# Kernel optimization log

Measured on AMD Instinct MI355X. Metric: run time of the kernel, lower is better.

## Reference

```python
import jax, jax.numpy as jnp
import numpy as np

NUM_NODES = 50000
IN_CH0 = 128
HEADS = 8
NUM_EDGES = 625000
IN_CH1 = 64


def setup_inputs() -> dict:
    key = jax.random.key(0)
    k0, k1, k2, k3 = jax.random.split(key, 4)
    x_0 = jax.random.normal(k0, (NUM_NODES, IN_CH0), dtype=jnp.float32)
    adjacency_0 = jax.random.randint(k1, (2, NUM_EDGES), 0, NUM_NODES, dtype=jnp.int64)
    x_1 = jax.random.normal(k2, (NUM_EDGES, IN_CH1), dtype=jnp.float32)
    # Xavier-uniform with relu gain, shape (2*C, heads)
    gain = float(np.sqrt(2.0))
    fan_in, fan_out = 2 * IN_CH0, HEADS
    bound = gain * np.sqrt(6.0 / (fan_in + fan_out))
    att_parameter = jax.random.uniform(k3, (2 * IN_CH0, HEADS), minval=-bound, maxval=bound, dtype=jnp.float32)
    return {"x_0": x_0, "adjacency_0": adjacency_0, "x_1": x_1, "att_parameter": att_parameter}


def reference(x_0, adjacency_0, x_1, att_parameter):
    # LiftLayer: gather source/target node feats, concat, small matmul, relu.
    source = adjacency_0[0]
    target = adjacency_0[1]
    C = x_0.shape[1]
    # cat(x_src, x_tgt) @ W  ==  x_src @ W[:C] + x_tgt @ W[C:]  (avoids materializing concat)
    edge_signal = jnp.einsum('ec,ch->eh', x_0[source], att_parameter[:C]) \
                + jnp.einsum('ec,ch->eh', x_0[target], att_parameter[C:])
    edge_signal = jax.nn.relu(edge_signal)  # [E, heads]
    # readout 'cat' is identity; dropout p=0.0 is identity (eval).
    return jnp.concatenate([edge_signal, x_1], axis=1)  # [E, heads + in_channels_1]
```

## Files before the change

### kernel.cpp

```cpp
#include <hip/hip_runtime.h>
#include <hip/hip_bf16.h>


#define NUM_NODES 50000
#define C0 128
#define HEADS 8
#define NODES_PER_BLK 16
#define XS_STRIDE 132

__global__ __launch_bounds__(256) void node_proj_kernel(
    const float* __restrict__ x0, const float* __restrict__ W,
    float* __restrict__ y, int num_nodes)
{
    __shared__ float Ws[2 * C0 * HEADS];
    __shared__ float xs[NODES_PER_BLK * XS_STRIDE];

    for (int i = threadIdx.x; i < 2 * C0 * HEADS; i += 256) Ws[i] = W[i];

    const int nodeBase = blockIdx.x * NODES_PER_BLK;
    for (int i = threadIdx.x; i < NODES_PER_BLK * C0; i += 256) {
        int r = i >> 7;
        int c = i & (C0 - 1);
        int n = nodeBase + r;
        xs[r * XS_STRIDE + c] = (n < num_nodes) ? x0[n * C0 + c] : 0.f;
    }
    __syncthreads();

    const int local = threadIdx.x >> 4;
    const int slot  = threadIdx.x & 15;
    const int half  = slot >> 3;
    const int h     = slot & 7;

    const float* xr = &xs[local * XS_STRIDE];
    const float* Wr = &Ws[half * C0 * HEADS + h];

    float acc = 0.f;
    #pragma unroll 8
    for (int c = 0; c < C0; ++c)
        acc = fmaf(xr[c], Wr[c * HEADS], acc);

    const int n = nodeBase + local;
    if (n < num_nodes) y[n * 16 + slot] = acc;
}

__global__ __launch_bounds__(256) void edge_out_kernel(
    const float* __restrict__ y, const float* __restrict__ x1,
    const int* __restrict__ adj, float* __restrict__ out, int E)
{
    const float4* __restrict__ yv  = (const float4*)y;
    const float4* __restrict__ x1v = (const float4*)x1;
    float4* __restrict__ outv = (float4*)out;

    const int total = E * 18;
    for (int i = blockIdx.x * blockDim.x + threadIdx.x; i < total;
         i += gridDim.x * blockDim.x) {
        const int e = i / 18;
        const int j = i - e * 18;
        float4 v;
        if (j >= 2) {
            v = x1v[e * 16 + (j - 2)];
        } else {
            const int s = adj[e];
            const int t = adj[E + e];
            const float4 a = yv[s * 4 + j];
            const float4 b = yv[t * 4 + 2 + j];
            v.x = fmaxf(a.x + b.x, 0.f);
            v.y = fmaxf(a.y + b.y, 0.f);
            v.z = fmaxf(a.z + b.z, 0.f);
            v.w = fmaxf(a.w + b.w, 0.f);
        }
        outv[i] = v;
    }
}

extern "C" void kernel_launch(void* const* d_in, const int* in_sizes, int n_in,
                              void* d_out, int out_size, void* d_ws, size_t ws_size,
                              hipStream_t stream) {
    const float* x0  = (const float*)d_in[0];
    const int*   adj = (const int*)d_in[1];
    const float* x1  = (const float*)d_in[2];
    const float* W   = (const float*)d_in[3];
    float* out = (float*)d_out;
    float* y   = (float*)d_ws;

    const int E = in_sizes[1] / 2;

    {
        dim3 grid((NUM_NODES + NODES_PER_BLK - 1) / NODES_PER_BLK);
        node_proj_kernel<<<grid, 256, 0, stream>>>(x0, W, y, NUM_NODES);
    }
    {
        const int total4 = E * 18;
        int blocks = (total4 + 255) / 256;
        if (blocks > 8192) blocks = 8192;
        edge_out_kernel<<<blocks, 256, 0, stream>>>(y, x1, adj, out, E);
    }
}
```

Before: 102.9 us.

## Compute edge heads per-thread into shared memory, then stream coalesced output

```diff
diff --git a/kernel.cpp b/kernel.cpp
--- a/kernel.cpp
+++ b/kernel.cpp
@@ -7,6 +7,7 @@
 #define HEADS 8
 #define NODES_PER_BLK 16
 #define XS_STRIDE 132
+#define EPB 256
 
 __global__ __launch_bounds__(256) void node_proj_kernel(
     const float* __restrict__ x0, const float* __restrict__ W,
@@ -51,25 +52,43 @@
     const float4* __restrict__ x1v = (const float4*)x1;
     float4* __restrict__ outv = (float4*)out;
 
-    const int total = E * 18;
-    for (int i = blockIdx.x * blockDim.x + threadIdx.x; i < total;
-         i += gridDim.x * blockDim.x) {
-        const int e = i / 18;
-        const int j = i - e * 18;
-        float4 v;
-        if (j >= 2) {
-            v = x1v[e * 16 + (j - 2)];
-        } else {
-            const int s = adj[e];
-            const int t = adj[E + e];
-            const float4 a = yv[s * 4 + j];
-            const float4 b = yv[t * 4 + 2 + j];
-            v.x = fmaxf(a.x + b.x, 0.f);
-            v.y = fmaxf(a.y + b.y, 0.f);
-            v.z = fmaxf(a.z + b.z, 0.f);
-            v.w = fmaxf(a.w + b.w, 0.f);
-        }
-        outv[i] = v;
+    __shared__ float4 head[EPB][2];
+
+    const int be  = blockIdx.x * EPB;
+    const int tid = threadIdx.x;
+
+    const int e = be + tid;
+    if (e < E) {
+        const int s = adj[e];
+        const int t = adj[E + e];
+        const float4 a0 = yv[s * 4 + 0];
+        const float4 a1 = yv[s * 4 + 1];
+        const float4 b0 = yv[t * 4 + 2];
+        const float4 b1 = yv[t * 4 + 3];
+        float4 h0, h1;
+        h0.x = fmaxf(a0.x + b0.x, 0.f);
+        h0.y = fmaxf(a0.y + b0.y, 0.f);
+        h0.z = fmaxf(a0.z + b0.z, 0.f);
+        h0.w = fmaxf(a0.w + b0.w, 0.f);
+        h1.x = fmaxf(a1.x + b1.x, 0.f);
+        h1.y = fmaxf(a1.y + b1.y, 0.f);
+        h1.z = fmaxf(a1.z + b1.z, 0.f);
+        h1.w = fmaxf(a1.w + b1.w, 0.f);
+        head[tid][0] = h0;
+        head[tid][1] = h1;
+    }
+    __syncthreads();
+
+    const int n   = (E - be < EPB) ? (E - be) : EPB;
+    const int n4  = n * 18;
+    const float4* __restrict__ x1b  = x1v  + (size_t)be * 16;
+    float4* __restrict__       outb = outv + (size_t)be * 18;
+
+    for (int i = tid; i < n4; i += 256) {
+        const int el = i / 18;
+        const int j  = i - el * 18;
+        const float4 v = (j >= 2) ? x1b[el * 16 + (j - 2)] : head[el][j];
+        outb[i] = v;
     }
 }
 
@@ -90,9 +109,7 @@
         node_proj_kernel<<<grid, 256, 0, stream>>>(x0, W, y, NUM_NODES);
     }
     {
-        const int total4 = E * 18;
-        int blocks = (total4 + 255) / 256;
-        if (blocks > 8192) blocks = 8192;
-        edge_out_kernel<<<blocks, 256, 0, stream>>>(y, x1, adj, out, E);
+        dim3 grid((E + EPB - 1) / EPB);
+        edge_out_kernel<<<grid, 256, 0, stream>>>(y, x1, adj, out, E);
     }
 }
```

New measurement: 110.6 us. 1.08x slower.

## Split edge kernel into head compute and streaming merge with split y layout

Applied to the files above, without the earlier changes.

```diff
diff --git a/kernel.cpp b/kernel.cpp
--- a/kernel.cpp
+++ b/kernel.cpp
@@ -1,12 +1,16 @@
 #include <hip/hip_runtime.h>
 #include <hip/hip_bf16.h>
 
+
+typedef float f4v __attribute__((ext_vector_type(4)));
 
 #define NUM_NODES 50000
 #define C0 128
 #define HEADS 8
 #define NODES_PER_BLK 16
 #define XS_STRIDE 132
+#define MGRID 2048
+#define MBLK 256
 
 __global__ __launch_bounds__(256) void node_proj_kernel(
     const float* __restrict__ x0, const float* __restrict__ W,
@@ -40,37 +44,68 @@
         acc = fmaf(xr[c], Wr[c * HEADS], acc);
 
     const int n = nodeBase + local;
-    if (n < num_nodes) y[n * 16 + slot] = acc;
+    if (n < num_nodes) y[half * (NUM_NODES * HEADS) + n * HEADS + h] = acc;
 }
 
-__global__ __launch_bounds__(256) void edge_out_kernel(
-    const float* __restrict__ y, const float* __restrict__ x1,
-    const int* __restrict__ adj, float* __restrict__ out, int E)
+static __device__ __forceinline__ f4v relu4(f4v a, f4v b) {
+    f4v r;
+    r.x = fmaxf(a.x + b.x, 0.f);
+    r.y = fmaxf(a.y + b.y, 0.f);
+    r.z = fmaxf(a.z + b.z, 0.f);
+    r.w = fmaxf(a.w + b.w, 0.f);
+    return r;
+}
+
+__global__ __launch_bounds__(256) void head_kernel(
+    const float* __restrict__ y, const int* __restrict__ adj,
+    float* __restrict__ hd, int E)
 {
-    const float4* __restrict__ yv  = (const float4*)y;
-    const float4* __restrict__ x1v = (const float4*)x1;
-    float4* __restrict__ outv = (float4*)out;
+    const int e = blockIdx.x * 256 + threadIdx.x;
+    if (e >= E) return;
+    const f4v* __restrict__ y0v = (const f4v*)y;
+    const f4v* __restrict__ y1v = y0v + 2 * NUM_NODES;
+    f4v* __restrict__ hdv = (f4v*)hd;
 
-    const int total = E * 18;
-    for (int i = blockIdx.x * blockDim.x + threadIdx.x; i < total;
-         i += gridDim.x * blockDim.x) {
-        const int e = i / 18;
-        const int j = i - e * 18;
-        float4 v;
-        if (j >= 2) {
-            v = x1v[e * 16 + (j - 2)];
-        } else {
-            const int s = adj[e];
-            const int t = adj[E + e];
-            const float4 a = yv[s * 4 + j];
-            const float4 b = yv[t * 4 + 2 + j];
-            v.x = fmaxf(a.x + b.x, 0.f);
-            v.y = fmaxf(a.y + b.y, 0.f);
-            v.z = fmaxf(a.z + b.z, 0.f);
-            v.w = fmaxf(a.w + b.w, 0.f);
-        }
-        outv[i] = v;
+    const int s = adj[e];
+    const int t = adj[E + e];
+    const f4v h0 = relu4(y0v[s * 2],     y1v[t * 2]);
+    const f4v h1 = relu4(y0v[s * 2 + 1], y1v[t * 2 + 1]);
+    hdv[e * 2]     = h0;
+    hdv[e * 2 + 1] = h1;
+}
+
+static __device__ __forceinline__ f4v merge_ld(
+    const f4v* __restrict__ hdv, const f4v* __restrict__ x1v, int i)
+{
+    const int e = i / 18;
+    const int j = i - e * 18;
+    const f4v* p = (j < 2) ? (hdv + (e * 2 + j)) : (x1v + (e * 16 + (j - 2)));
+    return *p;
+}
+
+__global__ __launch_bounds__(MBLK) void merge_kernel(
+    const float* __restrict__ hd, const float* __restrict__ x1,
+    float* __restrict__ out, int total)
+{
+    const f4v* __restrict__ hdv = (const f4v*)hd;
+    const f4v* __restrict__ x1v = (const f4v*)x1;
+    f4v* __restrict__ outv = (f4v*)out;
+
+    const int stride = MGRID * MBLK;
+    int i = blockIdx.x * MBLK + threadIdx.x;
+
+    for (; i + 3 * stride < total; i += 4 * stride) {
+        const f4v v0 = merge_ld(hdv, x1v, i);
+        const f4v v1 = merge_ld(hdv, x1v, i + stride);
+        const f4v v2 = merge_ld(hdv, x1v, i + 2 * stride);
+        const f4v v3 = merge_ld(hdv, x1v, i + 3 * stride);
+        outv[i]              = v0;
+        outv[i + stride]     = v1;
+        outv[i + 2 * stride] = v2;
+        outv[i + 3 * stride] = v3;
     }
+    for (; i < total; i += stride)
+        outv[i] = merge_ld(hdv, x1v, i);
 }
 
 extern "C" void kernel_launch(void* const* d_in, const int* in_sizes, int n_in,
@@ -82,6 +117,7 @@
     const float* W   = (const float*)d_in[3];
     float* out = (float*)d_out;
     float* y   = (float*)d_ws;
+    float* hd  = (float*)d_ws + 2 * NUM_NODES * HEADS;
 
     const int E = in_sizes[1] / 2;
 
@@ -90,9 +126,11 @@
         node_proj_kernel<<<grid, 256, 0, stream>>>(x0, W, y, NUM_NODES);
     }
     {
-        const int total4 = E * 18;
-        int blocks = (total4 + 255) / 256;
-        if (blocks > 8192) blocks = 8192;
-        edge_out_kernel<<<blocks, 256, 0, stream>>>(y, x1, adj, out, E);
+        dim3 grid((E + 255) / 256);
+        head_kernel<<<grid, 256, 0, stream>>>(y, adj, hd, E);
+    }
+    {
+        const int total = E * 18;
+        merge_kernel<<<MGRID, MBLK, 0, stream>>>(hd, x1, out, total);
     }
 }
```

New measurement: 114.3 us. +11.2%, slower.
